# Kernel tuning notes

Hardware: AMD Instinct MI355X
Metric: run time of the kernel (lower is better)

## Reference

```python
import jax, jax.numpy as jnp
import numpy as np
import math

IMAGE_C = 1
IMAGE_W = 28
PIXELS_PER_ROW = IMAGE_W * IMAGE_C
NUM_HEADS = 8
TOP_K = 96
WINDOW_SIZE = 128
NEG_INF = -jnp.inf


def _causal_2d_mask(T):
    idx = jnp.arange(T)
    q_i = (idx // PIXELS_PER_ROW)[:, None]
    q_j = (idx % PIXELS_PER_ROW // IMAGE_C)[:, None]
    q_c = (idx % IMAGE_C)[:, None]
    k_i = (idx // PIXELS_PER_ROW)[None, :]
    k_j = (idx % PIXELS_PER_ROW // IMAGE_C)[None, :]
    k_c = (idx % IMAGE_C)[None, :]
    allowed = (k_i < q_i) | ((k_i == q_i) & (k_j < q_j)) | ((k_i == q_i) & (k_j == q_j) & (k_c <= q_c))
    return jnp.where(allowed, 0.0, NEG_INF)[None, None]  # [1,1,T,T]


def _window_mask(T, window_size):
    idx = jnp.arange(T)
    blocked = idx[None, :] < idx[:, None] - window_size + 1
    return jnp.where(blocked, NEG_INF, 0.0)[None, None]  # [1,1,T,T]


def setup_inputs() -> dict:
    key = jax.random.key(0)
    ks = jax.random.split(key, 10)
    B, T, E = 4, 2048, 512
    H = NUM_HEADS
    s = 0.02
    return {
        "x": jax.random.normal(ks[0], (B, T, E), jnp.float32),
        "Wq": jax.random.normal(ks[1], (E, E), jnp.float32) * s,
        "bq": jnp.zeros((E,), jnp.float32),
        "Wk": jax.random.normal(ks[2], (E, E), jnp.float32) * s,
        "bk": jnp.zeros((E,), jnp.float32),
        "Wv": jax.random.normal(ks[3], (E, E), jnp.float32) * s,
        "bv": jnp.zeros((E,), jnp.float32),
        "Wo": jax.random.normal(ks[4], (E, E), jnp.float32) * s,
        "bo": jnp.zeros((E,), jnp.float32),
        "log_sigma": jnp.full((H, 1, 1), math.log(2.5), jnp.float32),
    }


def reference(x, Wq, bq, Wk, bk, Wv, bv, Wo, bo, log_sigma):
    B, T, E = x.shape
    H = NUM_HEADS
    D = E // H

    def split_heads(y):  # [B,T,E] -> [B,H,T,D]
        return y.reshape(B, T, H, D).transpose(0, 2, 1, 3)

    q = split_heads(x @ Wq.T + bq)
    k = split_heads(x @ Wk.T + bk)
    v = split_heads(x @ Wv.T + bv)

    # Gaussian-kernel (squared-distance) scores: ||q-k||^2 / (-2 sigma^2)
    q_sq = jnp.sum(q * q, axis=-1, keepdims=True)            # [B,H,T,1]
    k_sq = jnp.sum(k * k, axis=-1, keepdims=True).transpose(0, 1, 3, 2)  # [B,H,1,T]
    product = jnp.einsum("bhqd,bhkd->bhqk", q, k)
    dist_sq = q_sq + k_sq - 2.0 * product
    sigma_sq = jnp.exp(2.0 * log_sigma)                       # [H,1,1]
    scores = dist_sq / (-2.0 * sigma_sq)

    scores = scores + _causal_2d_mask(T)
    if WINDOW_SIZE < T:
        scores = scores + _window_mask(T, WINDOW_SIZE)

    if TOP_K < T:
        K_val = min(TOP_K, T)
        # keep only the top-K scores per row (threshold at the K-th value);
        # equivalent to torch's gather/scatter for distinct finite scores
        top_vals = jax.lax.top_k(scores, K_val)[0]            # [B,H,T,K]
        kth = top_vals[..., -1:]
        scores = jnp.where(scores >= kth, scores, NEG_INF)

    probs = jax.nn.softmax(scores, axis=-1)                   # dropout = identity (eval)
    out = jnp.einsum("bhqk,bhkd->bhqd", probs, v)
    out = out.transpose(0, 2, 1, 3).reshape(B, T, E)
    return out @ Wo.T + bo
```

## Files before the change

kernel.cpp:

```cpp
#include <hip/hip_runtime.h>
#include <math.h>

#define T_SEQ   2048
#define EDIM    512
#define NHEADS  8
#define DHEAD   64
#define BATCH   4
#define WIN     128
#define TOPK    96

typedef _Float16 f16;
typedef f16 f16x2 __attribute__((ext_vector_type(2)));
typedef f16 f16x4 __attribute__((ext_vector_type(4)));
typedef f16 f16x8 __attribute__((ext_vector_type(8)));
typedef float f32x4 __attribute__((ext_vector_type(4)));

#define GLD_LDS(gp, lp) \
    __builtin_amdgcn_global_load_lds((const __attribute__((address_space(1))) void*)(gp), \
                                     (__attribute__((address_space(3))) void*)(lp), 16, 0, 0)

__global__ __launch_bounds__(256) void convert_all(
    const float* __restrict__ x,  const float* __restrict__ wq,
    const float* __restrict__ wk, const float* __restrict__ wv,
    const float* __restrict__ wo,
    f16* __restrict__ xh, f16* __restrict__ wqkvh, f16* __restrict__ woh)
{
    long i = ((long)blockIdx.x * 256 + threadIdx.x) * 4;
    const float* src; f16* dst; long off;
    if      (i < 4194304L) { src = x;  dst = xh;             off = i;            }
    else if (i < 4456448L) { src = wq; dst = wqkvh;          off = i - 4194304L; }
    else if (i < 4718592L) { src = wk; dst = wqkvh + 262144; off = i - 4456448L; }
    else if (i < 4980736L) { src = wv; dst = wqkvh + 524288; off = i - 4718592L; }
    else                   { src = wo; dst = woh;            off = i - 4980736L; }
    float4 v = *(const float4*)(src + off);
    f16x4 h; h.x = (f16)v.x; h.y = (f16)v.y; h.z = (f16)v.z; h.w = (f16)v.w;
    *(f16x4*)(dst + off) = h;
}

__global__ __launch_bounds__(256) void gemm_qkv(
    const f16* __restrict__ A, const f16* __restrict__ W,
    const float* __restrict__ b0, const float* __restrict__ b1,
    const float* __restrict__ b2,
    f16* __restrict__ cq, f16* __restrict__ ck, f16* __restrict__ cv)
{
    __shared__ f16 SH[16384];
    f16* Ash = SH;
    f16* Bsh = SH + 8192;

    const int m0   = blockIdx.x * 128;
    const int n0   = blockIdx.y * 128;

    const int tid  = threadIdx.x;
    const int w    = tid >> 6;
    const int lane = tid & 63;
    const int K    = 512;
    const int lr   = lane & 15;
    const int lk8  = (lane >> 4) * 8;

    f32x4 acc[4][4];
#pragma unroll
    for (int i = 0; i < 4; i++)
#pragma unroll
        for (int j = 0; j < 4; j++) acc[i][j] = (f32x4){0.f, 0.f, 0.f, 0.f};

    const int wmi = (w & 1) * 4;
    const int wni = (w >> 1) * 4;

    for (int k0 = 0; k0 < K; k0 += 64) {
#pragma unroll
        for (int cc = 0; cc < 4; cc++) {
            const int c  = w * 4 + cc;
            const int ms = c & 7, kp = c >> 3;
            const int kcol = k0 + kp * 32 + lk8;
            GLD_LDS(A + (size_t)(m0 + ms * 16 + lr) * K + kcol, Ash + c * 512);
            GLD_LDS(W + (size_t)(n0 + ms * 16 + lr) * K + kcol, Bsh + c * 512);
        }
        __syncthreads();

#pragma unroll
        for (int kp = 0; kp < 2; kp++) {
            f16x8 af[4], bf[4];
#pragma unroll
            for (int i = 0; i < 4; i++)
                af[i] = *(const f16x8*)(Ash + (kp * 8 + wmi + i) * 512 + lane * 8);
#pragma unroll
            for (int j = 0; j < 4; j++)
                bf[j] = *(const f16x8*)(Bsh + (kp * 8 + wni + j) * 512 + lane * 8);
#pragma unroll
            for (int i = 0; i < 4; i++)
#pragma unroll
                for (int j = 0; j < 4; j++)
                    acc[i][j] = __builtin_amdgcn_mfma_f32_16x16x32_f16(af[i], bf[j], acc[i][j], 0, 0, 0);
        }
        __syncthreads();
    }

    const int quad = lane >> 4;
    const int mat  = n0 >> 9;
    const float* bias = (mat == 0) ? b0 : ((mat == 1) ? b1 : b2);
    const int bb  = m0 >> 11;
    const int t0  = m0 & (T_SEQ - 1);
    const int hh0 = (n0 & 511) >> 6;

    if (mat < 2) {
#pragma unroll
        for (int i = 0; i < 4; i++) {
#pragma unroll
            for (int j = 0; j < 4; j++) {
                const int nl = (w >> 1) * 64 + j * 16 + lr;
                const float bvv = bias[(n0 & 511) + nl];
#pragma unroll
                for (int r = 0; r < 4; r++) {
                    const int ml = (w & 1) * 64 + i * 16 + quad * 4 + r;
                    SH[ml * 128 + (nl ^ (((ml >> 2) & 7) << 4))] = (f16)(acc[i][j][r] + bvv);
                }
            }
        }
        __syncthreads();
        f16* dst = (mat == 0) ? cq : ck;
#pragma unroll
        for (int s = 0; s < 8; s++) {
            const int c   = tid + 256 * s;
            const int row = c >> 4;
            const int nt  = (c & 15) * 8;
            const f16x8 vv = *(const f16x8*)&SH[row * 128 + (nt ^ (((row >> 2) & 7) << 4))];
            const int hh = hh0 + (nt >> 6);
            const int dd = nt & 63;
            *(f16x8*)(dst + ((size_t)((bb * NHEADS + hh) * T_SEQ) + t0 + row) * 64 + dd) = vv;
        }
    } else {
#pragma unroll
        for (int i = 0; i < 4; i++) {
#pragma unroll
            for (int j = 0; j < 4; j++) {
                const int nl = (w >> 1) * 64 + j * 16 + lr;
                const float bvv = bias[(n0 & 511) + nl];
                const int mlb = (w & 1) * 64 + i * 16 + quad * 4;
                f16x4 pk;
#pragma unroll
                for (int r = 0; r < 4; r++) pk[r] = (f16)(acc[i][j][r] + bvv);
                *(f16x4*)&SH[nl * 128 + ((mlb + 8 * (nl & 15)) & 127)] = pk;
            }
        }
        __syncthreads();
#pragma unroll
        for (int s = 0; s < 8; s++) {
            const int c    = tid + 256 * s;
            const int nrow = c >> 4;
            const int cht  = c & 15;
            const int chl  = (cht + (nrow & 15)) & 15;
            const f16x8 vv = *(const f16x8*)&SH[nrow * 128 + chl * 8];
            const int hh = hh0 + (nrow >> 6);
            const int dd = nrow & 63;
            *(f16x8*)(cv + ((size_t)((bb * NHEADS + hh) * 64 + dd)) * T_SEQ + t0 + cht * 8) = vv;
        }
    }
}

__global__ __launch_bounds__(256) void gemm_o(
    const f16* __restrict__ A, const f16* __restrict__ W,
    const float* __restrict__ bias, float* __restrict__ C)
{
    __shared__ f16 Ash[16 * 512];
    __shared__ f16 Bsh[8 * 512];

    const int m0   = blockIdx.x * 128;
    const int n0   = blockIdx.y * 64;

    const int tid  = threadIdx.x;
    const int w    = tid >> 6;
    const int lane = tid & 63;
    const int lr   = lane & 15;
    const int lk8  = (lane >> 4) * 8;

    f32x4 acc[4][2];
#pragma unroll
    for (int i = 0; i < 4; i++)
#pragma unroll
        for (int j = 0; j < 2; j++) acc[i][j] = (f32x4){0.f, 0.f, 0.f, 0.f};

    for (int k0 = 0; k0 < 512; k0 += 64) {
#pragma unroll
        for (int cc = 0; cc < 4; cc++) {
            const int c  = w * 4 + cc;
            const int ms = c & 7, kp = c >> 3;
            GLD_LDS(A + (size_t)(m0 + ms * 16 + lr) * 512 + k0 + kp * 32 + lk8, Ash + c * 512);
        }
#pragma unroll
        for (int cc = 0; cc < 2; cc++) {
            const int c  = w * 2 + cc;
            const int ns = c & 3, kp = c >> 2;
            GLD_LDS(W + (size_t)(n0 + ns * 16 + lr) * 512 + k0 + kp * 32 + lk8, Bsh + c * 512);
        }
        __syncthreads();

#pragma unroll
        for (int kp = 0; kp < 2; kp++) {
            f16x8 af[4], bf[2];
#pragma unroll
            for (int i = 0; i < 4; i++)
                af[i] = *(const f16x8*)(Ash + (kp * 8 + (w & 1) * 4 + i) * 512 + lane * 8);
#pragma unroll
            for (int j = 0; j < 2; j++)
                bf[j] = *(const f16x8*)(Bsh + (kp * 4 + (w >> 1) * 2 + j) * 512 + lane * 8);
#pragma unroll
            for (int i = 0; i < 4; i++)
#pragma unroll
                for (int j = 0; j < 2; j++)
                    acc[i][j] = __builtin_amdgcn_mfma_f32_16x16x32_f16(af[i], bf[j], acc[i][j], 0, 0, 0);
        }
        __syncthreads();
    }

    const int quad = lane >> 4;
#pragma unroll
    for (int i = 0; i < 4; i++) {
#pragma unroll
        for (int j = 0; j < 2; j++) {
            const int n  = n0 + (w >> 1) * 32 + j * 16 + lr;
            const float bv = bias[n];
#pragma unroll
            for (int r = 0; r < 4; r++) {
                const int m = m0 + (w & 1) * 64 + i * 16 + quad * 4 + r;
                C[(size_t)m * 512 + n] = acc[i][j][r] + bv;
            }
        }
    }
}

__global__ __launch_bounds__(512, 4) void attn_v6(
    const f16* __restrict__ qh, const f16* __restrict__ kh,
    const f16* __restrict__ vtg, const float* __restrict__ logsig,
    f16* __restrict__ abh)
{
    __shared__ __align__(16) char smem[79616];
    f16*   Qs   = (f16*)smem;
    f16*   Ks   = (f16*)(smem + 11264);
    f16*   P    = (f16*)smem;
    float* Sc   = (float*)(smem + 45056);
    f16*   Vt   = (f16*)(smem + 45056);
    float* ksqs = (float*)(smem + 78848);

    const int tid = threadIdx.x, w = tid >> 6, lane = tid & 63;
    const int lr = lane & 15, quad = lane >> 4;
    const int q0 = blockIdx.x * 64, bh = blockIdx.y;
    const int h = bh & 7, b = bh >> 3;
    const size_t tb = (size_t)bh * T_SEQ;
    const int ks0 = q0 - 128;

    f16x8 vpre[3];
    int vd[3], vch[3];
#pragma unroll
    for (int s = 0; s < 3; s++) {
        const int i = tid + 512 * s;
        vd[s] = i / 24; vch[s] = i % 24;
        const int t0 = ks0 + vch[s] * 8;
        f16x8 vv = {};
        if (t0 >= 0) vv = *(const f16x8*)(vtg + ((size_t)bh * 64 + vd[s]) * T_SEQ + t0);
        vpre[s] = vv;
    }

    {
        const int row = tid >> 3, ch = tid & 7;
        f16x8 v = *(const f16x8*)(qh + (tb + q0 + row) * 64 + ch * 8);
        *(f16x8*)(Qs + row * 88 + ch * 8) = v;
    }
#pragma unroll
    for (int s = 0; s < 3; s++) {
        const int i = tid + 512 * s;
        const int row = i >> 3, ch = i & 7;
        const int kg = ks0 + row;
        f16x8 v = {};
        if (kg >= 0) v = *(const f16x8*)(kh + (tb + kg) * 64 + ch * 8);
        *(f16x8*)(Ks + row * 88 + ch * 8) = v;
        float ps = 0.f;
#pragma unroll
        for (int j = 0; j < 8; j++) { const float fv = (float)v[j]; ps += fv * fv; }
        ps += __shfl_xor(ps, 1);
        ps += __shfl_xor(ps, 2);
        ps += __shfl_xor(ps, 4);
        if (ch == 0) ksqs[row] = ps;
    }
    __syncthreads();

    const int mt  = w & 3;
    const int kh2 = w >> 2;
    f32x4 accQ[6];
#pragma unroll
    for (int jt = 0; jt < 6; jt++) accQ[jt] = (f32x4){0.f, 0.f, 0.f, 0.f};

#pragma unroll
    for (int kp = 0; kp < 2; kp++) {
        const f16x8 af = *(const f16x8*)(Qs + (mt * 16 + lr) * 88 + kp * 32 + quad * 8);
#pragma unroll
        for (int jt = 0; jt < 6; jt++) {
            const f16x8 bf = *(const f16x8*)(Ks + (kh2 * 96 + jt * 16 + lr) * 88 + kp * 32 + quad * 8);
            accQ[jt] = __builtin_amdgcn_mfma_f32_16x16x32_f16(af, bf, accQ[jt], 0, 0, 0);
        }
    }
    const float inv_s2 = __expf(-2.0f * logsig[h]);
#pragma unroll
    for (int jt = 0; jt < 6; jt++) {
        const int c  = kh2 * 96 + jt * 16 + lr;
        const float kq = ksqs[c];
        const int kg = ks0 + c;
#pragma unroll
        for (int r = 0; r < 4; r++) {
            const int dq = mt * 16 + quad * 4 + r;
            const unsigned wc = (unsigned)(c - dq - 1);
            if (wc < 128u) {
                Sc[dq * 132 + wc] = (kg >= 0) ? (accQ[jt][r] - 0.5f * kq) * inv_s2
                                              : -INFINITY;
            }
        }
    }
    __syncthreads();

    const int wq8 = w * 8;
#pragma unroll 1
    for (int g = 0; g < 2; g++) {
        const int dq0 = wq8 + g * 4;
        float s0[4], s1[4], m[4];
        unsigned u0[4], u1[4], t[4];
#pragma unroll
        for (int qq = 0; qq < 4; qq++) {
            const int dq = dq0 + qq;
            s0[qq] = Sc[dq * 132 + lane];
            s1[qq] = Sc[dq * 132 + 64 + lane];
            const unsigned b0 = __float_as_uint(s0[qq]);
            const unsigned b1 = __float_as_uint(s1[qq]);
            u0[qq] = b0 ^ (unsigned)(((int)b0 >> 31) | 0x80000000);
            u1[qq] = b1 ^ (unsigned)(((int)b1 >> 31) | 0x80000000);
            m[qq] = __uint_as_float(__builtin_amdgcn_readlane(__float_as_uint(s1[qq]), 63));
            t[qq] = 0u;
        }
#pragma unroll
        for (int bit = 31; bit >= 0; bit--) {
#pragma unroll
            for (int qq = 0; qq < 4; qq++) {
                const unsigned c = t[qq] | (1u << bit);
                const int n = __popcll(__ballot(u0[qq] >= c)) +
                              __popcll(__ballot(u1[qq] >= c));
                if (n >= TOPK) t[qq] = c;
            }
        }
#pragma unroll
        for (int qq = 0; qq < 4; qq++) {
            const int dq = dq0 + qq;
            const float p0 = (u0[qq] >= t[qq]) ? __expf(s0[qq] - m[qq]) : 0.f;
            const float p1 = (u1[qq] >= t[qq]) ? __expf(s1[qq] - m[qq]) : 0.f;
            P[dq * 216 + dq + 1 + lane]  = (f16)p0;
            P[dq * 216 + dq + 65 + lane] = (f16)p1;
            P[dq * 216 + ((lane <= dq) ? lane : lane + 128)] = (f16)0.f;
        }
    }
    __syncthreads();

#pragma unroll
    for (int s = 0; s < 3; s++)
        *(f16x8*)(Vt + vd[s] * 216 + vch[s] * 8) = vpre[s];
    __syncthreads();

    const int nh = w >> 2;
    f32x4 accO[2];
#pragma unroll
    for (int nt = 0; nt < 2; nt++) accO[nt] = (f32x4){0.f, 0.f, 0.f, 0.f};
    f32x4 accS = (f32x4){0.f, 0.f, 0.f, 0.f};
    f16x8 onesf;
#pragma unroll
    for (int j = 0; j < 8; j++) onesf[j] = (f16)1.0f;

#pragma unroll
    for (int ks = 0; ks < 6; ks++) {
        const f16x8 pf = *(const f16x8*)(P + (mt * 16 + lr) * 216 + ks * 32 + quad * 8);
#pragma unroll
        for (int nt = 0; nt < 2; nt++) {
            const f16x8 vf = *(const f16x8*)(Vt + (nh * 32 + nt * 16 + lr) * 216 + ks * 32 + quad * 8);
            accO[nt] = __builtin_amdgcn_mfma_f32_16x16x32_f16(pf, vf, accO[nt], 0, 0, 0);
        }
        accS = __builtin_amdgcn_mfma_f32_16x16x32_f16(pf, onesf, accS, 0, 0, 0);
    }
    float inv[4];
#pragma unroll
    for (int r = 0; r < 4; r++) inv[r] = 1.0f / accS[r];

#pragma unroll
    for (int nt = 0; nt < 2; nt++) {
        const int d = nh * 32 + nt * 16 + lr;
#pragma unroll
        for (int r = 0; r < 4; r++) {
            const int q = q0 + mt * 16 + quad * 4 + r;
            abh[((size_t)(b * T_SEQ + q)) * 512 + h * 64 + d] = (f16)(accO[nt][r] * inv[r]);
        }
    }
}

extern "C" void kernel_launch(void* const* d_in, const int* in_sizes, int n_in,
                              void* d_out, int out_size, void* d_ws, size_t ws_size,
                              hipStream_t stream)
{
    const float* x      = (const float*)d_in[0];
    const float* Wq     = (const float*)d_in[1];
    const float* bq     = (const float*)d_in[2];
    const float* Wk     = (const float*)d_in[3];
    const float* bk     = (const float*)d_in[4];
    const float* Wv     = (const float*)d_in[5];
    const float* bv     = (const float*)d_in[6];
    const float* Wo     = (const float*)d_in[7];
    const float* bo     = (const float*)d_in[8];
    const float* logsig = (const float*)d_in[9];

    f16* xh    = (f16*)d_ws;
    f16* wqkvh = xh + 4194304;
    f16* woh   = wqkvh + 786432;
    f16* qh    = woh + 262144;
    f16* kh    = qh + 4194304;
    f16* vtg   = kh + 4194304;
    f16* abh   = xh;

    convert_all<<<5120, 256, 0, stream>>>(x, Wq, Wk, Wv, Wo, xh, wqkvh, woh);

    gemm_qkv<<<dim3(64, 12), 256, 0, stream>>>(xh, wqkvh, bq, bk, bv, qh, kh, vtg);

    attn_v6<<<dim3(T_SEQ / 64, BATCH * NHEADS), 512, 0, stream>>>(
        qh, kh, vtg, logsig, abh);

    gemm_o<<<dim3(64, 8), 256, 0, stream>>>(abh, woh, bo, (float*)d_out);
}
```

Measured before the change: 174.7 us.

## Shrink attention tiles to 32 queries and load Q/K fragments directly from global

The attention kernel now handles 32 query rows per 256-thread block instead of 64 per 512-thread block, so each block spans 160 key columns instead of 192 and computes fewer wasted MFMA tiles. Q and K fragments are read straight from global memory into MFMA operands rather than staged in LDS, and the key norms are computed by per-row loops. LDS use drops to about 36KB, which should let more blocks reside per CU. In exchange, overlapping key windows are re-read from global across more blocks, and the direct fragment loads are less coalesced.

```diff
diff --git a/kernel.cpp b/kernel.cpp
--- a/kernel.cpp
+++ b/kernel.cpp
@@ -228,89 +228,82 @@
     }
 }
 
-__global__ __launch_bounds__(512, 4) void attn_v6(
+__global__ __launch_bounds__(256, 4) void attn_v7(
     const f16* __restrict__ qh, const f16* __restrict__ kh,
     const f16* __restrict__ vtg, const float* __restrict__ logsig,
     f16* __restrict__ abh)
 {
-    __shared__ __align__(16) char smem[79616];
-    f16*   Qs   = (f16*)smem;
-    f16*   Ks   = (f16*)(smem + 11264);
+    __shared__ __align__(16) char smem[35968];
     f16*   P    = (f16*)smem;
-    float* Sc   = (float*)(smem + 45056);
-    f16*   Vt   = (f16*)(smem + 45056);
-    float* ksqs = (float*)(smem + 78848);
+    float* Sc   = (float*)(smem + 13824);
+    f16*   Vt   = (f16*)(smem + 13824);
+    float* ksqs = (float*)(smem + 35328);
 
     const int tid = threadIdx.x, w = tid >> 6, lane = tid & 63;
     const int lr = lane & 15, quad = lane >> 4;
-    const int q0 = blockIdx.x * 64, bh = blockIdx.y;
+    const int q0 = blockIdx.x * 32, bh = blockIdx.y;
     const int h = bh & 7, b = bh >> 3;
     const size_t tb = (size_t)bh * T_SEQ;
     const int ks0 = q0 - 128;
 
-    f16x8 vpre[3];
-    int vd[3], vch[3];
-#pragma unroll
-    for (int s = 0; s < 3; s++) {
-        const int i = tid + 512 * s;
-        vd[s] = i / 24; vch[s] = i % 24;
+    f16x8 vpre[5];
+    int vd[5], vch[5];
+#pragma unroll
+    for (int s = 0; s < 5; s++) {
+        const int i = tid + 256 * s;
+        vd[s] = i / 20; vch[s] = i % 20;
         const int t0 = ks0 + vch[s] * 8;
         f16x8 vv = {};
         if (t0 >= 0) vv = *(const f16x8*)(vtg + ((size_t)bh * 64 + vd[s]) * T_SEQ + t0);
         vpre[s] = vv;
     }
 
-    {
-        const int row = tid >> 3, ch = tid & 7;
-        f16x8 v = *(const f16x8*)(qh + (tb + q0 + row) * 64 + ch * 8);
-        *(f16x8*)(Qs + row * 88 + ch * 8) = v;
-    }
-#pragma unroll
-    for (int s = 0; s < 3; s++) {
-        const int i = tid + 512 * s;
-        const int row = i >> 3, ch = i & 7;
-        const int kg = ks0 + row;
-        f16x8 v = {};
-        if (kg >= 0) v = *(const f16x8*)(kh + (tb + kg) * 64 + ch * 8);
-        *(f16x8*)(Ks + row * 88 + ch * 8) = v;
-        float ps = 0.f;
-#pragma unroll
-        for (int j = 0; j < 8; j++) { const float fv = (float)v[j]; ps += fv * fv; }
-        ps += __shfl_xor(ps, 1);
-        ps += __shfl_xor(ps, 2);
-        ps += __shfl_xor(ps, 4);
-        if (ch == 0) ksqs[row] = ps;
+    if (tid < 160) {
+        const int kg = ks0 + 1 + tid;
+        float s = 0.f;
+        if (kg >= 0) {
+            const f16x8* kr = (const f16x8*)(kh + (tb + kg) * 64);
+#pragma unroll
+            for (int ch = 0; ch < 8; ch++) {
+                const f16x8 kv = kr[ch];
+#pragma unroll
+                for (int j = 0; j < 8; j++) { const float f = (float)kv[j]; s += f * f; }
+            }
+        }
+        ksqs[tid] = s;
+    }
+
+    const int mt  = w & 1;
+    const int kh2 = w >> 1;
+    f32x4 accQ[5];
+#pragma unroll
+    for (int jt = 0; jt < 5; jt++) accQ[jt] = (f32x4){0.f, 0.f, 0.f, 0.f};
+
+#pragma unroll
+    for (int kp = 0; kp < 2; kp++) {
+        const f16x8 af = *(const f16x8*)(qh + (tb + q0 + mt * 16 + lr) * 64 + kp * 32 + quad * 8);
+#pragma unroll
+        for (int jt = 0; jt < 5; jt++) {
+            const int kg = ks0 + 1 + kh2 * 80 + jt * 16 + lr;
+            const f16x8 bf = *(const f16x8*)(kh + (tb + kg) * 64 + kp * 32 + quad * 8);
+            accQ[jt] = __builtin_amdgcn_mfma_f32_16x16x32_f16(af, bf, accQ[jt], 0, 0, 0);
+        }
     }
     __syncthreads();
 
-    const int mt  = w & 3;
-    const int kh2 = w >> 2;
-    f32x4 accQ[6];
-#pragma unroll
-    for (int jt = 0; jt < 6; jt++) accQ[jt] = (f32x4){0.f, 0.f, 0.f, 0.f};
-
-#pragma unroll
-    for (int kp = 0; kp < 2; kp++) {
-        const f16x8 af = *(const f16x8*)(Qs + (mt * 16 + lr) * 88 + kp * 32 + quad * 8);
-#pragma unroll
-        for (int jt = 0; jt < 6; jt++) {
-            const f16x8 bf = *(const f16x8*)(Ks + (kh2 * 96 + jt * 16 + lr) * 88 + kp * 32 + quad * 8);
-            accQ[jt] = __builtin_amdgcn_mfma_f32_16x16x32_f16(af, bf, accQ[jt], 0, 0, 0);
-        }
-    }
     const float inv_s2 = __expf(-2.0f * logsig[h]);
 #pragma unroll
-    for (int jt = 0; jt < 6; jt++) {
-        const int c  = kh2 * 96 + jt * 16 + lr;
+    for (int jt = 0; jt < 5; jt++) {
+        const int c  = kh2 * 80 + jt * 16 + lr;
         const float kq = ksqs[c];
-        const int kg = ks0 + c;
+        const int kg = ks0 + 1 + c;
 #pragma unroll
         for (int r = 0; r < 4; r++) {
             const int dq = mt * 16 + quad * 4 + r;
-            const unsigned wc = (unsigned)(c - dq - 1);
-            if (wc < 128u) {
-                Sc[dq * 132 + wc] = (kg >= 0) ? (accQ[jt][r] - 0.5f * kq) * inv_s2
-                                              : -INFINITY;
+            const unsigned j = (unsigned)(c - dq);
+            if (j < 128u) {
+                Sc[dq * 132 + j] = (kg >= 0) ? (accQ[jt][r] - 0.5f * kq) * inv_s2
+                                             : -INFINITY;
             }
         }
     }
@@ -351,17 +344,18 @@
             const float p1 = (u1[qq] >= t[qq]) ? __expf(s1[qq] - m[qq]) : 0.f;
             P[dq * 216 + dq + 1 + lane]  = (f16)p0;
             P[dq * 216 + dq + 65 + lane] = (f16)p1;
-            P[dq * 216 + ((lane <= dq) ? lane : lane + 128)] = (f16)0.f;
+            if (lane < 33)
+                P[dq * 216 + ((lane <= dq) ? lane : lane + 128)] = (f16)0.f;
         }
     }
     __syncthreads();
 
 #pragma unroll
-    for (int s = 0; s < 3; s++)
-        *(f16x8*)(Vt + vd[s] * 216 + vch[s] * 8) = vpre[s];
+    for (int s = 0; s < 5; s++)
+        *(f16x8*)(Vt + vd[s] * 168 + vch[s] * 8) = vpre[s];
     __syncthreads();
 
-    const int nh = w >> 2;
+    const int nh = w >> 1;
     f32x4 accO[2];
 #pragma unroll
     for (int nt = 0; nt < 2; nt++) accO[nt] = (f32x4){0.f, 0.f, 0.f, 0.f};
@@ -371,11 +365,11 @@
     for (int j = 0; j < 8; j++) onesf[j] = (f16)1.0f;
 
 #pragma unroll
-    for (int ks = 0; ks < 6; ks++) {
+    for (int ks = 0; ks < 5; ks++) {
         const f16x8 pf = *(const f16x8*)(P + (mt * 16 + lr) * 216 + ks * 32 + quad * 8);
 #pragma unroll
         for (int nt = 0; nt < 2; nt++) {
-            const f16x8 vf = *(const f16x8*)(Vt + (nh * 32 + nt * 16 + lr) * 216 + ks * 32 + quad * 8);
+            const f16x8 vf = *(const f16x8*)(Vt + (nh * 32 + nt * 16 + lr) * 168 + ks * 32 + quad * 8);
             accO[nt] = __builtin_amdgcn_mfma_f32_16x16x32_f16(pf, vf, accO[nt], 0, 0, 0);
         }
         accS = __builtin_amdgcn_mfma_f32_16x16x32_f16(pf, onesf, accS, 0, 0, 0);
@@ -422,7 +416,7 @@
 
     gemm_qkv<<<dim3(64, 12), 256, 0, stream>>>(xh, wqkvh, bq, bk, bv, qh, kh, vtg);
 
-    attn_v6<<<dim3(T_SEQ / 64, BATCH * NHEADS), 512, 0, stream>>>(
+    attn_v7<<<dim3(T_SEQ / 32, BATCH * NHEADS), 256, 0, stream>>>(
         qh, kh, vtg, logsig, abh);
 
     gemm_o<<<dim3(64, 8), 256, 0, stream>>>(abh, woh, bo, (float*)d_out);
```

Result: no change. 177.0 us (+1.3%).
